# Kernel tuning notes

Hardware: AMD Instinct MI355X
Metric: run time of the kernel (lower is better)

Reference implementation:

```python
import jax, jax.numpy as jnp
import numpy as np

N_NODES = 50000
N_EDGES = 600000
N_RELS = 19
D_IN = 128
D_HID = 64
D_OUT = 2


def setup_inputs() -> dict:
    key = jax.random.key(0)
    ks = jax.random.split(key, 10)
    feat = jax.random.normal(ks[0], (N_NODES, D_IN), dtype=jnp.float32)
    src = jax.random.randint(ks[1], (N_EDGES,), 0, N_NODES)
    dst = jax.random.randint(ks[2], (N_EDGES,), 0, N_NODES)
    etype = jax.random.randint(ks[3], (N_EDGES,), 0, N_RELS)
    s1 = 1.0 / np.sqrt(D_IN)
    s2 = 1.0 / np.sqrt(D_HID)
    W1 = jax.random.normal(ks[4], (N_RELS, D_IN, D_HID), dtype=jnp.float32) * s1
    loop1 = jax.random.normal(ks[5], (D_IN, D_HID), dtype=jnp.float32) * s1
    b1 = jnp.zeros((D_HID,), dtype=jnp.float32)
    W2 = jax.random.normal(ks[6], (N_RELS, D_HID, D_OUT), dtype=jnp.float32) * s2
    loop2 = jax.random.normal(ks[7], (D_HID, D_OUT), dtype=jnp.float32) * s2
    b2 = jnp.zeros((D_OUT,), dtype=jnp.float32)
    return {"feat": feat, "W1": W1, "loop1": loop1, "b1": b1,
            "W2": W2, "loop2": loop2, "b2": b2,
            "src": src, "dst": dst, "etype": etype}


def _rel_graph_conv(h, W, loop_w, bias, src, dst, etype, activation):
    # Per-relation transform of all nodes: [N, R, O]; then gather per edge.
    # (num_rels * out_feat is small, so this is cheaper than gathering W per edge.)
    transformed = jnp.einsum('nd,rdo->nro', h, W)
    msg = transformed[src, etype]                      # [E, O] edge messages
    agg = jax.ops.segment_sum(msg, dst, num_segments=h.shape[0])  # scatter-add
    out = agg + h @ loop_w + bias                      # self-loop + bias
    if activation is not None:
        out = activation(out)
    return out


def reference(feat, W1, loop1, b1, W2, loop2, b2, src, dst, etype):
    h = _rel_graph_conv(feat, W1, loop1, b1, src, dst, etype, jax.nn.relu)
    h = _rel_graph_conv(h, W2, loop2, b2, src, dst, etype, None)
    return h
```

## Files before the change

### kernel.cpp

```cpp
#include <hip/hip_runtime.h>

#define N_NODES 50000
#define N_EDGES 600000
#define N_RELS  19
#define D_IN    128
#define D_HID   64
#define D_OUT   2
#define EDGE_TILES ((N_EDGES + 127) / 128 + N_RELS)
#define SL_BLOCKS  ((N_NODES + 63) / 64)
#define PREP_BLOCKS ((N_RELS * D_HID * D_IN + N_RELS * 16 * D_HID + D_HID * D_IN + 255) / 256)

typedef unsigned short u16;
typedef unsigned int   u32;
typedef __attribute__((ext_vector_type(8))) short sfrag;
typedef __attribute__((ext_vector_type(4))) float f32x4;

__device__ __forceinline__ u16 f2bf(float f){
  union { float f; u32 i; } v; v.f = f;
  u32 r = v.i + 0x7fffu + ((v.i >> 16) & 1u);
  return (u16)(r >> 16);
}
__device__ __forceinline__ float bf2f(u16 u){
  union { u32 i; float f; } v; v.i = ((u32)u) << 16; return v.f;
}

__global__ __launch_bounds__(256) void k_fused_pre(const float* __restrict__ feat,
                                                   u16* __restrict__ featb,
                                                   const int* __restrict__ et,
                                                   const int* __restrict__ dst,
                                                   int* __restrict__ hist_rel,
                                                   int* __restrict__ hist_dst){
  int i = blockIdx.x * 256 + threadIdx.x;
  float2 f = ((const float2*)feat)[i];
  ((u32*)featb)[i] = (u32)f2bf(f.x) | ((u32)f2bf(f.y) << 16);
  if (blockIdx.x < (N_EDGES + 255) / 256) {
    __shared__ int lh[N_RELS];
    int tid = threadIdx.x;
    if (tid < N_RELS) lh[tid] = 0;
    __syncthreads();
    int e = blockIdx.x * 256 + tid;
    if (e < N_EDGES) {
      atomicAdd(&lh[et[e]], 1);
      atomicAdd(&hist_dst[dst[e]], 1);
    }
    __syncthreads();
    if (tid < N_RELS && lh[tid]) atomicAdd(&hist_rel[tid], lh[tid]);
  }
}

__global__ __launch_bounds__(256) void k_alloc_scan(
    const int* __restrict__ hist_dst, int* __restrict__ dstart,
    int* __restrict__ cur_dst, int* __restrict__ gcnt,
    const int* __restrict__ hist_rel, int* __restrict__ offs,
    int* __restrict__ toff, int* __restrict__ cur_rel,
    const float* __restrict__ W1, const float* __restrict__ loop1,
    const float* __restrict__ W2, u16* __restrict__ W1Tb,
    u16* __restrict__ loop1Tb, u16* __restrict__ W2Tb){
  if (blockIdx.x >= 197) {
    int idx = (blockIdx.x - 197) * 256 + threadIdx.x;
    const int T1 = N_RELS * D_HID * D_IN;
    const int T2 = T1 + N_RELS * 16 * D_HID;
    const int T3 = T2 + D_HID * D_IN;
    if (idx < T1) {
      int r = idx / (D_HID * D_IN);
      int t = idx - r * (D_HID * D_IN);
      int j = t >> 7, d = t & 127;
      W1Tb[idx] = f2bf(W1[(r * D_IN + d) * D_HID + j]);
    } else if (idx < T2) {
      int k2 = idx - T1;
      int r = k2 / (16 * D_HID);
      int t = k2 - r * (16 * D_HID);
      int n = t >> 6, k = t & 63;
      W2Tb[k2] = (n < D_OUT) ? f2bf(W2[(r * D_HID + k) * D_OUT + n]) : (u16)0;
    } else if (idx < T3) {
      int k2 = idx - T2;
      int j = k2 >> 7, d = k2 & 127;
      loop1Tb[k2] = f2bf(loop1[d * D_HID + j]);
    }
    return;
  }
  if (blockIdx.x == 196) {
    if (threadIdx.x == 0) {
      int acc = 0, tacc = 0;
      offs[0] = 0; toff[0] = 0;
      for (int r = 0; r < N_RELS; ++r) {
        cur_rel[r] = acc;
        int c = hist_rel[r];
        acc += c;                offs[r + 1] = acc;
        tacc += (c + 127) >> 7;  toff[r + 1] = tacc;
      }
    }
    return;
  }
  __shared__ int wbase[4];
  int tid = threadIdx.x, lane = tid & 63, wv = tid >> 6;
  int n = blockIdx.x * 256 + tid;
  int v = (n < N_NODES) ? hist_dst[n] : 0;
  int x = v;
  #pragma unroll
  for (int o = 1; o < 64; o <<= 1) { int u = __shfl_up(x, o); if (lane >= o) x += u; }
  if (lane == 63) wbase[wv] = atomicAdd(gcnt, x);
  __syncthreads();
  int start = wbase[wv] + x - v;
  if (n < N_NODES) { dstart[n] = start; cur_dst[n] = start; }
}

__global__ __launch_bounds__(256) void k_scatter_rel(const int* __restrict__ et,
                                                     int* __restrict__ cursor,
                                                     int* __restrict__ perm){
  __shared__ int lh[N_RELS], base[N_RELS];
  int tid = threadIdx.x;
  if (tid < N_RELS) lh[tid] = 0;
  __syncthreads();
  int e = blockIdx.x * 256 + tid;
  int r = 0, my = 0;
  bool valid = e < N_EDGES;
  if (valid) { r = et[e]; my = atomicAdd(&lh[r], 1); }
  __syncthreads();
  if (tid < N_RELS && lh[tid]) base[tid] = atomicAdd(&cursor[tid], lh[tid]);
  __syncthreads();
  if (valid) perm[base[r] + my] = e;
}

__global__ __launch_bounds__(256) void k_se1(
    const u16* __restrict__ featb, const u16* __restrict__ W1Tb,
    const u16* __restrict__ loop1Tb, const float* __restrict__ b1,
    const int* __restrict__ src, const int* __restrict__ dst,
    const int* __restrict__ perm, const int* __restrict__ offs,
    const int* __restrict__ toff, int* __restrict__ cur_dst,
    u16* __restrict__ msgbuf, float* __restrict__ agg1f){
  __shared__ __align__(16) u16 Als[128][136];
  __shared__ __align__(16) u16 Bls[64][136];
  __shared__ int posIds[128];
  int tid = threadIdx.x, lane = tid & 63, w = tid >> 6;
  int r16 = lane & 15, c4 = lane >> 4;

  if (blockIdx.x >= EDGE_TILES) {
    int base = (blockIdx.x - EDGE_TILES) * 64;
    { int j = tid >> 2, seg = tid & 3;
      const uint4* g = (const uint4*)(loop1Tb + j * 128) + seg * 4;
      uint4* d = (uint4*)&Bls[j][seg * 32];
      d[0] = g[0]; d[1] = g[1]; d[2] = g[2]; d[3] = g[3]; }
    { int i = tid >> 2, seg = tid & 3;
      int n = base + i; if (n >= N_NODES) n = N_NODES - 1;
      const uint4* g = (const uint4*)(featb + (size_t)n * D_IN) + seg * 4;
      uint4* d = (uint4*)&Als[i][seg * 32];
      d[0] = g[0]; d[1] = g[1]; d[2] = g[2]; d[3] = g[3]; }
    __syncthreads();
    sfrag aF[4];
    #pragma unroll
    for (int kk = 0; kk < 4; ++kk)
      aF[kk] = *(const sfrag*)&Als[w * 16 + r16][kk * 32 + c4 * 8];
    #pragma unroll
    for (int ct = 0; ct < 4; ++ct) {
      f32x4 acc = {0.f, 0.f, 0.f, 0.f};
      #pragma unroll
      for (int kk = 0; kk < 4; ++kk) {
        sfrag bF = *(const sfrag*)&Bls[ct * 16 + r16][kk * 32 + c4 * 8];
        acc = __builtin_amdgcn_mfma_f32_16x16x32_bf16(aF[kk], bF, acc, 0, 0, 0);
      }
      int col = ct * 16 + r16;
      float bias = b1[col];
      #pragma unroll
      for (int reg = 0; reg < 4; ++reg) {
        int row = base + w * 16 + c4 * 4 + reg;
        if (row < N_NODES) agg1f[(size_t)row * D_HID + col] = acc[reg] + bias;
      }
    }
    return;
  }

  int b = blockIdx.x;
  unsigned long long mm = __ballot((lane < N_RELS) && (b >= toff[lane + 1]));
  int rel = __popcll(mm);
  if (rel >= N_RELS) return;
  int ts = offs[rel] + ((b - toff[rel]) << 7);
  int vc = offs[rel + 1] - ts; if (vc > 128) vc = 128;

  {
    int j = tid >> 2, seg = tid & 3;
    const uint4* g = (const uint4*)(W1Tb + ((size_t)rel * 64 + j) * 128) + seg * 4;
    uint4* d = (uint4*)&Bls[j][seg * 32];
    d[0] = g[0]; d[1] = g[1]; d[2] = g[2]; d[3] = g[3];
  }
  #pragma unroll
  for (int p = 0; p < 2; ++p) {
    int i = p * 64 + (tid >> 2), seg = tid & 3;
    if (i < vc) {
      int e = perm[ts + i];
      if (seg == 0) posIds[i] = atomicAdd(&cur_dst[dst[e]], 1);
      const uint4* g = (const uint4*)(featb + (size_t)src[e] * D_IN) + seg * 4;
      uint4* d = (uint4*)&Als[i][seg * 32];
      d[0] = g[0]; d[1] = g[1]; d[2] = g[2]; d[3] = g[3];
    } else if (seg == 0) posIds[i] = -1;
  }
  __syncthreads();

  sfrag aF[2][4];
  #pragma unroll
  for (int mt = 0; mt < 2; ++mt)
    #pragma unroll
    for (int kk = 0; kk < 4; ++kk)
      aF[mt][kk] = *(const sfrag*)&Als[w * 32 + mt * 16 + r16][kk * 32 + c4 * 8];
  f32x4 accAll[2][4];
  #pragma unroll
  for (int ct = 0; ct < 4; ++ct) {
    sfrag bF[4];
    #pragma unroll
    for (int kk = 0; kk < 4; ++kk)
      bF[kk] = *(const sfrag*)&Bls[ct * 16 + r16][kk * 32 + c4 * 8];
    #pragma unroll
    for (int mt = 0; mt < 2; ++mt) {
      f32x4 acc = {0.f, 0.f, 0.f, 0.f};
      #pragma unroll
      for (int kk = 0; kk < 4; ++kk)
        acc = __builtin_amdgcn_mfma_f32_16x16x32_bf16(aF[mt][kk], bF[kk], acc, 0, 0, 0);
      accAll[mt][ct] = acc;
    }
  }
  float* msg = (float*)&Als[0][0];
  #pragma unroll
  for (int mt = 0; mt < 2; ++mt)
    #pragma unroll
    for (int ct = 0; ct < 4; ++ct) {
      int col = ct * 16 + r16;
      #pragma unroll
      for (int reg = 0; reg < 4; ++reg) {
        int row = w * 32 + mt * 16 + c4 * 4 + reg;
        msg[row * 68 + col] = accAll[mt][ct][reg];
      }
    }
  __syncthreads();
  { int row = tid >> 1, half = tid & 1;
    int pos = posIds[row];
    if (pos >= 0) {
      const float* mr = msg + row * 68 + half * 32;
      u32 pk[16];
      #pragma unroll
      for (int q = 0; q < 16; ++q)
        pk[q] = (u32)f2bf(mr[2 * q]) | ((u32)f2bf(mr[2 * q + 1]) << 16);
      uint4* d = (uint4*)(msgbuf + (size_t)pos * D_HID + half * 32);
      d[0] = *(uint4*)&pk[0];  d[1] = *(uint4*)&pk[4];
      d[2] = *(uint4*)&pk[8];  d[3] = *(uint4*)&pk[12];
    } }
}

__global__ __launch_bounds__(256) void k_agg_relu_self2(
    const u16* __restrict__ msgbuf, const int* __restrict__ dstart,
    const int* __restrict__ cnt, const float* __restrict__ agg1f,
    const float* __restrict__ loop2, const float* __restrict__ b2,
    u16* __restrict__ h1b, float* __restrict__ out){
  int wv = threadIdx.x >> 6, lane = threadIdx.x & 63;
  int n = blockIdx.x * 4 + wv;
  int s = dstart[n], epos = s + cnt[n];
  int h = lane >> 5, c = lane & 31;
  float a0 = 0.f, a1 = 0.f;
  for (int i = s + h; i < epos; i += 2) {
    u32 v = ((const u32*)msgbuf)[(size_t)i * 32 + c];
    a0 += bf2f((u16)(v & 0xffffu));
    a1 += bf2f((u16)(v >> 16));
  }
  a0 += __shfl_down(a0, 32);
  a1 += __shfl_down(a1, 32);
  float p0 = 0.f, p1 = 0.f;
  if (h == 0) {
    float2 sl = ((const float2*)(agg1f + (size_t)n * D_HID))[c];
    float v0 = a0 + sl.x, v1 = a1 + sl.y;
    v0 = v0 > 0.f ? v0 : 0.f;
    v1 = v1 > 0.f ? v1 : 0.f;
    ((u32*)h1b)[(size_t)n * 32 + c] = (u32)f2bf(v0) | ((u32)f2bf(v1) << 16);
    float2 w0 = ((const float2*)loop2)[2 * c];
    float2 w1 = ((const float2*)loop2)[2 * c + 1];
    p0 = v0 * w0.x + v1 * w1.x;
    p1 = v0 * w0.y + v1 * w1.y;
  }
  #pragma unroll
  for (int off = 16; off; off >>= 1) {
    p0 += __shfl_down(p0, off);
    p1 += __shfl_down(p1, off);
  }
  if (lane == 0) {
    out[n * 2]     = p0 + b2[0];
    out[n * 2 + 1] = p1 + b2[1];
  }
}

__global__ __launch_bounds__(256) void k_edge2_mfma(
    const u16* __restrict__ h1b, const u16* __restrict__ W2Tb,
    const int* __restrict__ src, const int* __restrict__ dst,
    const int* __restrict__ perm, const int* __restrict__ offs,
    const int* __restrict__ toff, float* __restrict__ out){
  __shared__ __align__(16) u16 Als[128][72];
  __shared__ __align__(16) u16 Bls[16][72];
  __shared__ int dstIds[128];
  int tid = threadIdx.x, lane = tid & 63, w = tid >> 6;

  int b = blockIdx.x;
  unsigned long long mm = __ballot((lane < N_RELS) && (b >= toff[lane + 1]));
  int rel = __popcll(mm);
  if (rel >= N_RELS) return;
  int ts = offs[rel] + ((b - toff[rel]) << 7);
  int vc = offs[rel + 1] - ts; if (vc > 128) vc = 128;

  if (tid < 128) {
    ((uint4*)&Bls[tid >> 3][0])[tid & 7] = ((const uint4*)(W2Tb + (size_t)rel * 16 * 64))[tid];
  }
  {
    int i = tid >> 1, half = tid & 1;
    if (i < vc) {
      int e = perm[ts + i];
      if (half == 0) dstIds[i] = dst[e];
      const uint4* g = (const uint4*)(h1b + (size_t)src[e] * D_HID) + half * 4;
      uint4* d = (uint4*)&Als[i][half * 32];
      d[0] = g[0]; d[1] = g[1]; d[2] = g[2]; d[3] = g[3];
    } else if (half == 0) dstIds[i] = -1;
  }
  __syncthreads();

  int r16 = lane & 15, c4 = lane >> 4;
  #pragma unroll
  for (int mt = 0; mt < 2; ++mt) {
    f32x4 acc = {0.f, 0.f, 0.f, 0.f};
    #pragma unroll
    for (int kk = 0; kk < 2; ++kk) {
      sfrag aF = *(const sfrag*)&Als[w * 32 + mt * 16 + r16][kk * 32 + c4 * 8];
      sfrag bF = *(const sfrag*)&Bls[r16][kk * 32 + c4 * 8];
      acc = __builtin_amdgcn_mfma_f32_16x16x32_bf16(aF, bF, acc, 0, 0, 0);
    }
    if (r16 < D_OUT) {
      #pragma unroll
      for (int reg = 0; reg < 4; ++reg) {
        int row = w * 32 + mt * 16 + c4 * 4 + reg;
        int dn = dstIds[row];
        if (dn >= 0) atomicAdd(&out[dn * D_OUT + r16], acc[reg]);
      }
    }
  }
}

extern "C" void kernel_launch(void* const* d_in, const int* in_sizes, int n_in,
                              void* d_out, int out_size, void* d_ws, size_t ws_size,
                              hipStream_t stream){
  const float* feat  = (const float*)d_in[0];
  const float* W1    = (const float*)d_in[1];
  const float* loop1 = (const float*)d_in[2];
  const float* b1    = (const float*)d_in[3];
  const float* W2    = (const float*)d_in[4];
  const float* loop2 = (const float*)d_in[5];
  const float* b2    = (const float*)d_in[6];
  const int* src     = (const int*)d_in[7];
  const int* dst     = (const int*)d_in[8];
  const int* et      = (const int*)d_in[9];
  float* out = (float*)d_out;

  char* w = (char*)d_ws;
  u16*   W1Tb     = (u16*)(w);
  u16*   W2Tb     = (u16*)(w + 311296);
  u16*   loop1Tb  = (u16*)(w + 350208);
  int*   hist_rel = (int*)(w + 366592);
  int*   gcnt     = (int*)(w + 366720);
  int*   hist_dst = (int*)(w + 366848);
  int*   offs     = (int*)(w + 566848);
  int*   toff     = (int*)(w + 566976);
  int*   cur_rel  = (int*)(w + 567104);
  int*   dstart   = (int*)(w + 567232);
  int*   cur_dst  = (int*)(w + 767232);
  int*   perm     = (int*)(w + 967232);
  u16*   featb    = (u16*)(w + 3367232);
  float* agg1f    = (float*)(w + 16167232);
  u16*   h1b      = (u16*)(w + 28967232);
  u16*   msgbuf   = (u16*)(w + 35367232);

  hipMemsetAsync(w + 366592, 0, 200256, stream);
  k_fused_pre     <<<12500, 256, 0, stream>>>(feat, featb, et, dst, hist_rel, hist_dst);
  k_alloc_scan    <<<197 + PREP_BLOCKS, 256, 0, stream>>>(
                      hist_dst, dstart, cur_dst, gcnt, hist_rel, offs, toff, cur_rel,
                      W1, loop1, W2, W1Tb, loop1Tb, W2Tb);
  k_scatter_rel   <<<2344,  256, 0, stream>>>(et, cur_rel, perm);
  k_se1           <<<EDGE_TILES + SL_BLOCKS, 256, 0, stream>>>(
                      featb, W1Tb, loop1Tb, b1, src, dst, perm, offs, toff,
                      cur_dst, msgbuf, agg1f);
  k_agg_relu_self2<<<12500, 256, 0, stream>>>(msgbuf, dstart, hist_dst, agg1f,
                                              loop2, b2, h1b, out);
  k_edge2_mfma    <<<EDGE_TILES, 256, 0, stream>>>(h1b, W2Tb, src, dst, perm, offs, toff, out);
}
```

Measured before the change: 316.9 us.

## Precompute per-node layer-2 transforms for all relations, gather per edge; direct-load A fragments

Layer 2 is restructured to first compute every node's 64x38 transform for all relations with one MFMA pass, storing it in a float table that reuses the featb workspace. A simple per-edge kernel then gathers a float2 and atomically adds it to the output, replacing the per-relation edge tiles that gathered 64-wide h1 rows. In layer 1, A fragments are now loaded straight from global memory into registers instead of staging through LDS. Messages are packed to bf16 in registers before going to LDS, which shrinks the LDS footprint. The cost is an extra launch and a 50000x40 float intermediate, in exchange for much less gather traffic per edge.

```diff
diff --git a/kernel.cpp b/kernel.cpp
--- a/kernel.cpp
+++ b/kernel.cpp
@@ -8,7 +8,8 @@
 #define D_OUT   2
 #define EDGE_TILES ((N_EDGES + 127) / 128 + N_RELS)
 #define SL_BLOCKS  ((N_NODES + 63) / 64)
-#define PREP_BLOCKS ((N_RELS * D_HID * D_IN + N_RELS * 16 * D_HID + D_HID * D_IN + 255) / 256)
+#define PREP_ELEMS (N_RELS * D_HID * D_IN + 48 * 64 + D_HID * D_IN)
+#define PREP_BLOCKS ((PREP_ELEMS + 255) / 256)
 
 typedef unsigned short u16;
 typedef unsigned int   u32;
@@ -55,25 +56,28 @@
     int* __restrict__ toff, int* __restrict__ cur_rel,
     const float* __restrict__ W1, const float* __restrict__ loop1,
     const float* __restrict__ W2, u16* __restrict__ W1Tb,
-    u16* __restrict__ loop1Tb, u16* __restrict__ W2Tb){
+    u16* __restrict__ loop1Tb, u16* __restrict__ W2allT){
   if (blockIdx.x >= 197) {
     int idx = (blockIdx.x - 197) * 256 + threadIdx.x;
     const int T1 = N_RELS * D_HID * D_IN;
-    const int T2 = T1 + N_RELS * 16 * D_HID;
-    const int T3 = T2 + D_HID * D_IN;
+    const int T2c = T1 + 48 * 64;
+    const int T3 = T2c + D_HID * D_IN;
     if (idx < T1) {
       int r = idx / (D_HID * D_IN);
       int t = idx - r * (D_HID * D_IN);
       int j = t >> 7, d = t & 127;
       W1Tb[idx] = f2bf(W1[(r * D_IN + d) * D_HID + j]);
-    } else if (idx < T2) {
+    } else if (idx < T2c) {
       int k2 = idx - T1;
-      int r = k2 / (16 * D_HID);
-      int t = k2 - r * (16 * D_HID);
-      int n = t >> 6, k = t & 63;
-      W2Tb[k2] = (n < D_OUT) ? f2bf(W2[(r * D_HID + k) * D_OUT + n]) : (u16)0;
+      int n = k2 >> 6, k = k2 & 63;
+      float val = 0.f;
+      if (n < N_RELS * D_OUT) {
+        int r = n >> 1, o = n & 1;
+        val = W2[(r * D_HID + k) * D_OUT + o];
+      }
+      W2allT[k2] = f2bf(val);
     } else if (idx < T3) {
-      int k2 = idx - T2;
+      int k2 = idx - T2c;
       int j = k2 >> 7, d = k2 & 127;
       loop1Tb[k2] = f2bf(loop1[d * D_HID + j]);
     }
@@ -129,8 +133,8 @@
     const int* __restrict__ perm, const int* __restrict__ offs,
     const int* __restrict__ toff, int* __restrict__ cur_dst,
     u16* __restrict__ msgbuf, float* __restrict__ agg1f){
-  __shared__ __align__(16) u16 Als[128][136];
   __shared__ __align__(16) u16 Bls[64][136];
+  __shared__ __align__(16) u16 msg[128][72];
   __shared__ int posIds[128];
   int tid = threadIdx.x, lane = tid & 63, w = tid >> 6;
   int r16 = lane & 15, c4 = lane >> 4;
@@ -141,16 +145,12 @@
       const uint4* g = (const uint4*)(loop1Tb + j * 128) + seg * 4;
       uint4* d = (uint4*)&Bls[j][seg * 32];
       d[0] = g[0]; d[1] = g[1]; d[2] = g[2]; d[3] = g[3]; }
-    { int i = tid >> 2, seg = tid & 3;
-      int n = base + i; if (n >= N_NODES) n = N_NODES - 1;
-      const uint4* g = (const uint4*)(featb + (size_t)n * D_IN) + seg * 4;
-      uint4* d = (uint4*)&Als[i][seg * 32];
-      d[0] = g[0]; d[1] = g[1]; d[2] = g[2]; d[3] = g[3]; }
+    int arow = base + w * 16 + r16; if (arow >= N_NODES) arow = N_NODES - 1;
+    sfrag aF[4];
+    #pragma unroll
+    for (int kk = 0; kk < 4; ++kk)
+      aF[kk] = *(const sfrag*)(featb + (size_t)arow * D_IN + kk * 32 + c4 * 8);
     __syncthreads();
-    sfrag aF[4];
-    #pragma unroll
-    for (int kk = 0; kk < 4; ++kk)
-      aF[kk] = *(const sfrag*)&Als[w * 16 + r16][kk * 32 + c4 * 8];
     #pragma unroll
     for (int ct = 0; ct < 4; ++ct) {
       f32x4 acc = {0.f, 0.f, 0.f, 0.f};
@@ -163,8 +163,8 @@
       float bias = b1[col];
       #pragma unroll
       for (int reg = 0; reg < 4; ++reg) {
-        int row = base + w * 16 + c4 * 4 + reg;
-        if (row < N_NODES) agg1f[(size_t)row * D_HID + col] = acc[reg] + bias;
+        int orow = base + w * 16 + c4 * 4 + reg;
+        if (orow < N_NODES) agg1f[(size_t)orow * D_HID + col] = acc[reg] + bias;
       }
     }
     return;
@@ -177,32 +177,29 @@
   int ts = offs[rel] + ((b - toff[rel]) << 7);
   int vc = offs[rel + 1] - ts; if (vc > 128) vc = 128;
 
+  int myPos = -1;
+  if (tid < 128 && tid < vc) {
+    int e = perm[ts + tid];
+    myPos = atomicAdd(&cur_dst[dst[e]], 1);
+  }
   {
     int j = tid >> 2, seg = tid & 3;
     const uint4* g = (const uint4*)(W1Tb + ((size_t)rel * 64 + j) * 128) + seg * 4;
     uint4* d = (uint4*)&Bls[j][seg * 32];
     d[0] = g[0]; d[1] = g[1]; d[2] = g[2]; d[3] = g[3];
   }
-  #pragma unroll
-  for (int p = 0; p < 2; ++p) {
-    int i = p * 64 + (tid >> 2), seg = tid & 3;
-    if (i < vc) {
-      int e = perm[ts + i];
-      if (seg == 0) posIds[i] = atomicAdd(&cur_dst[dst[e]], 1);
-      const uint4* g = (const uint4*)(featb + (size_t)src[e] * D_IN) + seg * 4;
-      uint4* d = (uint4*)&Als[i][seg * 32];
-      d[0] = g[0]; d[1] = g[1]; d[2] = g[2]; d[3] = g[3];
-    } else if (seg == 0) posIds[i] = -1;
-  }
-  __syncthreads();
-
   sfrag aF[2][4];
   #pragma unroll
-  for (int mt = 0; mt < 2; ++mt)
+  for (int mt = 0; mt < 2; ++mt) {
+    int row = w * 32 + mt * 16 + r16;
+    int rr = row < vc ? row : vc - 1;
+    int s = src[perm[ts + rr]];
+    const u16* ap = featb + (size_t)s * D_IN + c4 * 8;
     #pragma unroll
     for (int kk = 0; kk < 4; ++kk)
-      aF[mt][kk] = *(const sfrag*)&Als[w * 32 + mt * 16 + r16][kk * 32 + c4 * 8];
-  f32x4 accAll[2][4];
+      aF[mt][kk] = *(const sfrag*)(ap + kk * 32);
+  }
+  __syncthreads();
   #pragma unroll
   for (int ct = 0; ct < 4; ++ct) {
     sfrag bF[4];
@@ -215,33 +212,28 @@
       #pragma unroll
       for (int kk = 0; kk < 4; ++kk)
         acc = __builtin_amdgcn_mfma_f32_16x16x32_bf16(aF[mt][kk], bF[kk], acc, 0, 0, 0);
-      accAll[mt][ct] = acc;
-    }
-  }
-  float* msg = (float*)&Als[0][0];
-  #pragma unroll
-  for (int mt = 0; mt < 2; ++mt)
-    #pragma unroll
-    for (int ct = 0; ct < 4; ++ct) {
-      int col = ct * 16 + r16;
       #pragma unroll
       for (int reg = 0; reg < 4; ++reg) {
-        int row = w * 32 + mt * 16 + c4 * 4 + reg;
-        msg[row * 68 + col] = accAll[mt][ct][reg];
-      }
-    }
+        float v = acc[reg];
+        float o = __shfl_xor(v, 1);
+        float lo = (lane & 1) ? o : v;
+        float hi = (lane & 1) ? v : o;
+        u32 pk = (u32)f2bf(lo) | ((u32)f2bf(hi) << 16);
+        if (!(lane & 1)) {
+          int orow = w * 32 + mt * 16 + c4 * 4 + reg;
+          *(u32*)&msg[orow][ct * 16 + r16] = pk;
+        }
+      }
+    }
+  }
+  if (tid < 128) posIds[tid] = myPos;
   __syncthreads();
   { int row = tid >> 1, half = tid & 1;
     int pos = posIds[row];
     if (pos >= 0) {
-      const float* mr = msg + row * 68 + half * 32;
-      u32 pk[16];
-      #pragma unroll
-      for (int q = 0; q < 16; ++q)
-        pk[q] = (u32)f2bf(mr[2 * q]) | ((u32)f2bf(mr[2 * q + 1]) << 16);
+      const uint4* mr = (const uint4*)&msg[row][half * 32];
       uint4* d = (uint4*)(msgbuf + (size_t)pos * D_HID + half * 32);
-      d[0] = *(uint4*)&pk[0];  d[1] = *(uint4*)&pk[4];
-      d[2] = *(uint4*)&pk[8];  d[3] = *(uint4*)&pk[12];
+      d[0] = mr[0]; d[1] = mr[1]; d[2] = mr[2]; d[3] = mr[3];
     } }
 }
 
@@ -285,57 +277,52 @@
   }
 }
 
-__global__ __launch_bounds__(256) void k_edge2_mfma(
-    const u16* __restrict__ h1b, const u16* __restrict__ W2Tb,
-    const int* __restrict__ src, const int* __restrict__ dst,
-    const int* __restrict__ perm, const int* __restrict__ offs,
-    const int* __restrict__ toff, float* __restrict__ out){
-  __shared__ __align__(16) u16 Als[128][72];
-  __shared__ __align__(16) u16 Bls[16][72];
-  __shared__ int dstIds[128];
+__global__ __launch_bounds__(256) void k_t2(
+    const u16* __restrict__ h1b, const u16* __restrict__ W2allT,
+    float* __restrict__ T2){
+  __shared__ __align__(16) u16 Bls[48][72];
   int tid = threadIdx.x, lane = tid & 63, w = tid >> 6;
-
-  int b = blockIdx.x;
-  unsigned long long mm = __ballot((lane < N_RELS) && (b >= toff[lane + 1]));
-  int rel = __popcll(mm);
-  if (rel >= N_RELS) return;
-  int ts = offs[rel] + ((b - toff[rel]) << 7);
-  int vc = offs[rel + 1] - ts; if (vc > 128) vc = 128;
-
-  if (tid < 128) {
-    ((uint4*)&Bls[tid >> 3][0])[tid & 7] = ((const uint4*)(W2Tb + (size_t)rel * 16 * 64))[tid];
-  }
-  {
-    int i = tid >> 1, half = tid & 1;
-    if (i < vc) {
-      int e = perm[ts + i];
-      if (half == 0) dstIds[i] = dst[e];
-      const uint4* g = (const uint4*)(h1b + (size_t)src[e] * D_HID) + half * 4;
-      uint4* d = (uint4*)&Als[i][half * 32];
-      d[0] = g[0]; d[1] = g[1]; d[2] = g[2]; d[3] = g[3];
-    } else if (half == 0) dstIds[i] = -1;
-  }
-  __syncthreads();
-
   int r16 = lane & 15, c4 = lane >> 4;
-  #pragma unroll
-  for (int mt = 0; mt < 2; ++mt) {
+  for (int idx = tid; idx < 48 * 8; idx += 256) {
+    int row = idx >> 3, q = idx & 7;
+    ((uint4*)&Bls[row][0])[q] = ((const uint4*)W2allT)[idx];
+  }
+  int base = blockIdx.x * 64;
+  int arow = base + w * 16 + r16; if (arow >= N_NODES) arow = N_NODES - 1;
+  sfrag aF[2];
+  #pragma unroll
+  for (int kk = 0; kk < 2; ++kk)
+    aF[kk] = *(const sfrag*)(h1b + (size_t)arow * D_HID + kk * 32 + c4 * 8);
+  __syncthreads();
+  #pragma unroll
+  for (int ct = 0; ct < 3; ++ct) {
     f32x4 acc = {0.f, 0.f, 0.f, 0.f};
     #pragma unroll
     for (int kk = 0; kk < 2; ++kk) {
-      sfrag aF = *(const sfrag*)&Als[w * 32 + mt * 16 + r16][kk * 32 + c4 * 8];
-      sfrag bF = *(const sfrag*)&Bls[r16][kk * 32 + c4 * 8];
-      acc = __builtin_amdgcn_mfma_f32_16x16x32_bf16(aF, bF, acc, 0, 0, 0);
-    }
-    if (r16 < D_OUT) {
+      sfrag bF = *(const sfrag*)&Bls[ct * 16 + r16][kk * 32 + c4 * 8];
+      acc = __builtin_amdgcn_mfma_f32_16x16x32_bf16(aF[kk], bF, acc, 0, 0, 0);
+    }
+    int col = ct * 16 + r16;
+    if (col < N_RELS * D_OUT) {
       #pragma unroll
       for (int reg = 0; reg < 4; ++reg) {
-        int row = w * 32 + mt * 16 + c4 * 4 + reg;
-        int dn = dstIds[row];
-        if (dn >= 0) atomicAdd(&out[dn * D_OUT + r16], acc[reg]);
-      }
-    }
-  }
+        int orow = base + w * 16 + c4 * 4 + reg;
+        if (orow < N_NODES) T2[(size_t)orow * 40 + col] = acc[reg];
+      }
+    }
+  }
+}
+
+__global__ __launch_bounds__(256) void k_edge2(
+    const float* __restrict__ T2, const int* __restrict__ src,
+    const int* __restrict__ dst, const int* __restrict__ et,
+    float* __restrict__ out){
+  int e = blockIdx.x * 256 + threadIdx.x;
+  if (e >= N_EDGES) return;
+  int s = src[e], d = dst[e], r = et[e];
+  float2 v = *(const float2*)(T2 + (size_t)s * 40 + r * 2);
+  atomicAdd(&out[d * 2],     v.x);
+  atomicAdd(&out[d * 2 + 1], v.y);
 }
 
 extern "C" void kernel_launch(void* const* d_in, const int* in_sizes, int n_in,
@@ -355,7 +342,7 @@
 
   char* w = (char*)d_ws;
   u16*   W1Tb     = (u16*)(w);
-  u16*   W2Tb     = (u16*)(w + 311296);
+  u16*   W2allT   = (u16*)(w + 311296);
   u16*   loop1Tb  = (u16*)(w + 350208);
   int*   hist_rel = (int*)(w + 366592);
   int*   gcnt     = (int*)(w + 366720);
@@ -367,6 +354,7 @@
   int*   cur_dst  = (int*)(w + 767232);
   int*   perm     = (int*)(w + 967232);
   u16*   featb    = (u16*)(w + 3367232);
+  float* T2f      = (float*)(w + 3367232);
   float* agg1f    = (float*)(w + 16167232);
   u16*   h1b      = (u16*)(w + 28967232);
   u16*   msgbuf   = (u16*)(w + 35367232);
@@ -375,12 +363,13 @@
   k_fused_pre     <<<12500, 256, 0, stream>>>(feat, featb, et, dst, hist_rel, hist_dst);
   k_alloc_scan    <<<197 + PREP_BLOCKS, 256, 0, stream>>>(
                       hist_dst, dstart, cur_dst, gcnt, hist_rel, offs, toff, cur_rel,
-                      W1, loop1, W2, W1Tb, loop1Tb, W2Tb);
+                      W1, loop1, W2, W1Tb, loop1Tb, W2allT);
   k_scatter_rel   <<<2344,  256, 0, stream>>>(et, cur_rel, perm);
   k_se1           <<<EDGE_TILES + SL_BLOCKS, 256, 0, stream>>>(
                       featb, W1Tb, loop1Tb, b1, src, dst, perm, offs, toff,
                       cur_dst, msgbuf, agg1f);
   k_agg_relu_self2<<<12500, 256, 0, stream>>>(msgbuf, dstart, hist_dst, agg1f,
                                               loop2, b2, h1b, out);
-  k_edge2_mfma    <<<EDGE_TILES, 256, 0, stream>>>(h1b, W2Tb, src, dst, perm, offs, toff, out);
-}
+  k_t2            <<<SL_BLOCKS, 256, 0, stream>>>(h1b, W2allT, T2f);
+  k_edge2         <<<(N_EDGES + 255) / 256, 256, 0, stream>>>(T2f, src, dst, et, out);
+}
```

After: 337.8 us. 1.07x slower.
